# Kernel optimization log

Measured on AMD Instinct MI355X. Metric: run time of the kernel, lower is better.

Reference implementation:

```python
import jax, jax.numpy as jnp
import numpy as np


def setup_inputs() -> dict:
    key = jax.random.key(0)
    kx, kw = jax.random.split(key)
    x = jax.random.normal(kx, (32, 2048, 256), dtype=jnp.float32)
    W = jax.random.normal(kw, (1024, 256), dtype=jnp.float32)  # codebook [K, D]
    return {"x": x, "W": W}


def reference(x, W):
    D = W.shape[1]
    flat = x.reshape(-1, D)  # [N, D]
    # Squared Euclidean distances [N, K]; argmin is identical to cdist argmin.
    d2 = (
        jnp.sum(flat * flat, axis=1, keepdims=True)
        - 2.0 * (flat @ W.T)
        + jnp.sum(W * W, axis=1)
    )
    idx = jnp.argmin(d2, axis=1)  # [N]
    quant = W[idx].reshape(x.shape)  # direct gather == one-hot @ W
    # Straight-through estimator
    quantized = x + jax.lax.stop_gradient(quant - x)
    e_latent = jnp.mean((jax.lax.stop_gradient(quantized) - x) ** 2)
    q_latent = jnp.mean((quantized - jax.lax.stop_gradient(x)) ** 2)
    commitment_cost = 0.25
    loss = q_latent + commitment_cost * e_latent
    return quantized, loss, idx[:, None]
```

## Files before the change

kernel.cpp:

```cpp
#include <hip/hip_runtime.h>


#define NROWS    65536
#define DDIM     256
#define KCODES   1024
#define DEXT     512
#define ND_TOTAL 16777216

typedef __attribute__((ext_vector_type(8))) short bf16x8;
typedef __attribute__((ext_vector_type(4))) float floatx4;

__device__ __forceinline__ unsigned short f2bf(float f) {
    unsigned int u = __float_as_uint(f);
    return (unsigned short)((u + 0x7FFFu + ((u >> 16) & 1u)) >> 16);
}
__device__ __forceinline__ float bf2f(unsigned short h) {
    return __uint_as_float((unsigned int)h << 16);
}
__device__ __forceinline__ void split4(float4 v, ushort4* hi, ushort4* lo) {
    unsigned short hx = f2bf(v.x), hy = f2bf(v.y), hz = f2bf(v.z), hw = f2bf(v.w);
    *hi = make_ushort4(hx, hy, hz, hw);
    *lo = make_ushort4(f2bf(v.x - bf2f(hx)), f2bf(v.y - bf2f(hy)),
                       f2bf(v.z - bf2f(hz)), f2bf(v.w - bf2f(hw)));
}
__device__ __forceinline__ void async_copy16(void* lds, const void* g) {
    __builtin_amdgcn_global_load_lds(
        (const __attribute__((address_space(1))) unsigned int*)g,
        (__attribute__((address_space(3))) unsigned int*)lds, 16, 0, 0);
}

__device__ __forceinline__ void merge2(float& v1, int& k1, float& v2, int& k2,
                                       float o1, int ok1, float o2, int ok2) {
    bool aw = (v1 < o1) || (v1 == o1 && k1 < ok1);
    float ca = aw ? v2 : v1; int kca = aw ? k2 : k1;
    float cb = aw ? o1 : o2; int kcb = aw ? ok1 : ok2;
    float nv1 = aw ? v1 : o1; int nk1 = aw ? k1 : ok1;
    bool cw = (ca < cb) || (ca == cb && kca < kcb);
    v1 = nv1; k1 = nk1;
    v2 = cw ? ca : cb; k2 = cw ? kca : kcb;
}

__global__ void vq_prepw(const float* __restrict__ W, unsigned short* __restrict__ What,
                         float* __restrict__ w2, float* __restrict__ w2m,
                         float* __restrict__ lossws) {
    int k = blockIdx.x * 256 + threadIdx.x;
    if (k == 0) lossws[0] = 0.0f;
    if (k >= KCODES) return;
    const float4* wr = (const float4*)(W + (size_t)k * DDIM);
    unsigned short* hrow = What + (size_t)k * DEXT;
    float s = 0.0f;
    for (int i = 0; i < 64; ++i) {
        float4 v = wr[i];
        s = fmaf(v.x, v.x, s); s = fmaf(v.y, v.y, s);
        s = fmaf(v.z, v.z, s); s = fmaf(v.w, v.w, s);
        ushort4 hv, lv;
        split4(v, &hv, &lv);
        *(ushort4*)(hrow + i * 4) = hv;
        *(ushort4*)(hrow + 256 + i * 4) = lv;
    }
    w2[k] = s;
    w2m[k] = s - 256.0f;
}

__global__ void vq_convx(const float* __restrict__ x, unsigned short* Xhat) {
    int gid = blockIdx.x * 256 + threadIdx.x;
    int row = gid >> 6, q = gid & 63;
    float4 v = ((const float4*)x)[gid];
    ushort4 hv, lv;
    split4(v, &hv, &lv);
    unsigned short* r = Xhat + (size_t)row * DEXT;
    *(ushort4*)(r + q * 4) = hv;
    *(ushort4*)(r + 256 + q * 4) = lv;
}

__global__ __launch_bounds__(256, 2) void vq_main(
    const unsigned short* Xhat, const unsigned short* __restrict__ What,
    const float* __restrict__ x, const float* __restrict__ W,
    const float* __restrict__ w2, const float* __restrict__ w2m,
    float* qout, float* lossws, float* idx_out)
{
    __shared__ __align__(16) unsigned short smem[2 * 4 * 128 * 32];
    __shared__ float Wm[KCODES];

    float* rv1   = (float*)smem;
    float* rv2   = rv1 + 256;
    int*   rk1   = (int*)(rv2 + 256);
    int*   rk2   = rk1 + 256;
    int*   candk = rk2 + 256;
    float* resc  = (float*)(candk + 512);
    int*   fink  = (int*)(resc + 512);

    const int tid  = threadIdx.x;
    const int wave = tid >> 6, lane = tid & 63;
    const int quad = lane >> 4, l15 = lane & 15;
    const int wr = wave >> 1, wc = wave & 1;
    const int row0 = blockIdx.x * 128;

    #pragma unroll
    for (int t = 0; t < 4; ++t) Wm[t * 256 + tid] = w2m[t * 256 + tid];

    float s1[16], s2[16];
    #pragma unroll
    for (int s = 0; s < 16; ++s) { s1[s] = 3.0e38f; s2[s] = 3.0e38f; }

    const int r0 = tid >> 2, p0 = tid & 3;
    const int psw = (p0 ^ ((r0 >> 1) & 3)) << 3;
    const int quadS8 = (quad ^ ((l15 >> 1) & 3)) << 3;
    const unsigned short* Ab = Xhat + (size_t)row0 * DEXT;

    auto STAGE = [&](int q, int cb) {
        const int ct = q >> 3, dc = (q & 7) << 5;
        const unsigned short* An = Ab + (size_t)r0 * DEXT + dc + psw;
        const unsigned short* Bn = What + ((size_t)(ct * 128 + r0)) * DEXT + dc + psw;
        unsigned short* L = smem + cb * 16384 + tid * 8;
        async_copy16(L,          An);
        async_copy16(L + 2048,   An + 64 * DEXT);
        async_copy16(L + 4096,   An + 256);
        async_copy16(L + 6144,   An + 64 * DEXT + 256);
        async_copy16(L + 8192,   Bn);
        async_copy16(L + 10240,  Bn + 64 * DEXT);
        async_copy16(L + 12288,  Bn + 256);
        async_copy16(L + 14336,  Bn + 64 * DEXT + 256);
    };

    STAGE(0, 0);
    STAGE(1, 1);

    floatx4 acc[4][4];
    #pragma unroll
    for (int i = 0; i < 4; ++i)
        #pragma unroll
        for (int j = 0; j < 4; ++j) acc[i][j] = (floatx4){0.f, 0.f, 0.f, 0.f};

    #pragma unroll 1
    for (int q = 0; q < 64; ++q) {
        const int cb = q & 1;
        if (q != 63) { asm volatile("s_waitcnt vmcnt(8)" ::: "memory"); }
        else         { asm volatile("s_waitcnt vmcnt(0)" ::: "memory"); }
        __builtin_amdgcn_s_barrier();
        asm volatile("" ::: "memory");
        __builtin_amdgcn_s_setprio(1);

        const unsigned short* Sb = smem + cb * 16384;
        bf16x8 a0[4], a1[4], b0[4], b1[4];
        #pragma unroll
        for (int i = 0; i < 4; ++i) {
            const int ro = (wr * 64 + i * 16 + l15) * 32 + quadS8;
            a0[i] = *(const bf16x8*)(Sb + ro);
            a1[i] = *(const bf16x8*)(Sb + 4096 + ro);
        }
        #pragma unroll
        for (int j = 0; j < 4; ++j) {
            const int ro = (wc * 64 + j * 16 + l15) * 32 + quadS8;
            b0[j] = *(const bf16x8*)(Sb + 8192 + ro);
            b1[j] = *(const bf16x8*)(Sb + 12288 + ro);
        }
        #pragma unroll
        for (int i = 0; i < 4; ++i)
            #pragma unroll
            for (int j = 0; j < 4; ++j) {
                acc[i][j] = __builtin_amdgcn_mfma_f32_16x16x32_bf16(a0[i], b0[j], acc[i][j], 0, 0, 0);
                acc[i][j] = __builtin_amdgcn_mfma_f32_16x16x32_bf16(a1[i], b1[j], acc[i][j], 0, 0, 0);
                acc[i][j] = __builtin_amdgcn_mfma_f32_16x16x32_bf16(a0[i], b1[j], acc[i][j], 0, 0, 0);
                acc[i][j] = __builtin_amdgcn_mfma_f32_16x16x32_bf16(a1[i], b0[j], acc[i][j], 0, 0, 0);
            }
        __builtin_amdgcn_s_setprio(0);
        asm volatile("s_waitcnt lgkmcnt(0)" ::: "memory");
        __builtin_amdgcn_s_barrier();
        asm volatile("" ::: "memory");
        if (q + 2 < 64) STAGE(q + 2, cb);

        if ((q & 7) == 7) {
            const int ctf = q >> 3;
            #pragma unroll
            for (int j = 0; j < 4; ++j) {
                int cc = ctf * 128 + wc * 64 + j * 16 + l15;
                float wm = Wm[cc];
                unsigned pay = (unsigned)((j << 3) | ctf);
                #pragma unroll
                for (int i = 0; i < 4; ++i)
                    #pragma unroll
                    for (int r = 0; r < 4; ++r) {
                        float v = fmaf(-2.0f, acc[i][j][r], wm);
                        float pf = __uint_as_float((__float_as_uint(v) & 0xFFFFFFE0u) | pay);
                        int s = i * 4 + r;
                        float t = fminf(s1[s], pf);
                        s2[s] = fminf(s2[s], fmaxf(s1[s], pf));
                        s1[s] = t;
                    }
            }
            #pragma unroll
            for (int i = 0; i < 4; ++i)
                #pragma unroll
                for (int j = 0; j < 4; ++j) acc[i][j] = (floatx4){0.f, 0.f, 0.f, 0.f};
        }
    }

    float v1[16], v2[16];
    int k1[16], k2[16];
    #pragma unroll
    for (int s = 0; s < 16; ++s) {
        unsigned u1 = __float_as_uint(s1[s]) & 31u;
        unsigned u2 = __float_as_uint(s2[s]) & 31u;
        v1[s] = s1[s]; v2[s] = s2[s];
        k1[s] = (int)(u1 & 7u) * 128 + wc * 64 + (int)(u1 >> 3) * 16 + l15;
        k2[s] = (int)(u2 & 7u) * 128 + wc * 64 + (int)(u2 >> 3) * 16 + l15;
    }
    #pragma unroll
    for (int m = 1; m < 16; m <<= 1) {
        #pragma unroll
        for (int s = 0; s < 16; ++s) {
            float o1 = __shfl_xor(v1[s], m, 64);
            int  ok1 = __shfl_xor(k1[s], m, 64);
            float o2 = __shfl_xor(v2[s], m, 64);
            int  ok2 = __shfl_xor(k2[s], m, 64);
            merge2(v1[s], k1[s], v2[s], k2[s], o1, ok1, o2, ok2);
        }
    }
    if (l15 == 0) {
        #pragma unroll
        for (int s = 0; s < 16; ++s) {
            int row = wr * 64 + (s >> 2) * 16 + quad * 4 + (s & 3);
            rv1[wc * 128 + row] = v1[s]; rk1[wc * 128 + row] = k1[s];
            rv2[wc * 128 + row] = v2[s]; rk2[wc * 128 + row] = k2[s];
        }
    }
    __syncthreads();
    if (tid < 128) {
        candk[tid * 4 + 0] = rk1[tid];
        candk[tid * 4 + 1] = rk2[tid];
        candk[tid * 4 + 2] = rk1[128 + tid];
        candk[tid * 4 + 3] = rk2[128 + tid];
    }
    __syncthreads();
    #pragma unroll
    for (int j2 = 0; j2 < 2; ++j2) {
        int job = tid + j2 * 256;
        int r = job >> 2, cn = job & 3;
        int k = candk[r * 4 + cn];
        const float4* xr  = (const float4*)(x + (size_t)(row0 + r) * DDIM);
        const float4* wrp = (const float4*)(W + (size_t)k * DDIM);
        float dot = 0.0f;
        #pragma unroll 8
        for (int i = 0; i < 64; ++i) {
            float4 va = xr[i], vb = wrp[i];
            dot = fmaf(va.x, vb.x, dot); dot = fmaf(va.y, vb.y, dot);
            dot = fmaf(va.z, vb.z, dot); dot = fmaf(va.w, vb.w, dot);
        }
        resc[r * 4 + cn] = fmaf(-2.0f, dot, w2[k]);
    }
    __syncthreads();
    if (tid < 128) {
        float bd = resc[tid * 4 + 0];
        int   bk = candk[tid * 4 + 0];
        #pragma unroll
        for (int cn = 1; cn < 4; ++cn) {
            float d = resc[tid * 4 + cn];
            int   k = candk[tid * 4 + cn];
            if (d < bd || (d == bd && k < bk)) { bd = d; bk = k; }
        }
        fink[tid] = bk;
        idx_out[row0 + tid] = (float)bk;
    }
    __syncthreads();

    const int c4 = tid & 63, rsub = tid >> 6;
    float lsum = 0.0f;
    for (int it2 = 0; it2 < 32; ++it2) {
        int r = it2 * 4 + rsub;
        int k = fink[r];
        float4 wv = ((const float4*)(W + (size_t)k * DDIM))[c4];
        float4 xv = ((const float4*)(x + (size_t)(row0 + r) * DDIM))[c4];
        ((float4*)(qout + (size_t)(row0 + r) * DDIM))[c4] = wv;
        float dx = wv.x - xv.x, dy = wv.y - xv.y;
        float dz = wv.z - xv.z, dw = wv.w - xv.w;
        lsum = fmaf(dx, dx, lsum); lsum = fmaf(dy, dy, lsum);
        lsum = fmaf(dz, dz, lsum); lsum = fmaf(dw, dw, lsum);
    }
    #pragma unroll
    for (int off = 32; off > 0; off >>= 1) lsum += __shfl_down(lsum, off, 64);
    if (lane == 0) atomicAdd(lossws, lsum);
}

__global__ void vq_fin(const float* __restrict__ lossws, float* __restrict__ loss_out) {
    loss_out[0] = 1.25f * lossws[0] / (float)ND_TOTAL;
}

extern "C" void kernel_launch(void* const* d_in, const int* in_sizes, int n_in,
                              void* d_out, int out_size, void* d_ws, size_t ws_size,
                              hipStream_t stream) {
    const float* x = (const float*)d_in[0];
    const float* W = (const float*)d_in[1];
    float* out = (float*)d_out;
    unsigned short* Xhat = (unsigned short*)d_out;
    unsigned short* What = (unsigned short*)d_ws;
    float* w2     = (float*)((char*)d_ws + (1 << 20));
    float* w2m    = w2 + 1024;
    float* lossws = w2 + 2048;
    float* idx_out = out + (size_t)ND_TOTAL + 1;

    vq_prepw<<<4, 256, 0, stream>>>(W, What, w2, w2m, lossws);
    vq_convx<<<16384, 256, 0, stream>>>(x, Xhat);
    vq_main<<<512, 256, 0, stream>>>(Xhat, What, x, W, w2, w2m, out, lossws, idx_out);
    vq_fin<<<1, 1, 0, stream>>>(lossws, out + ND_TOTAL);
}
```

Measured before the change: 336.2 us.

## Widen main block to 512 threads with 256-code tiles and fuse prep kernels

After: 405.1 us. 1.21x slower.

```diff
diff --git a/kernel.cpp b/kernel.cpp
--- a/kernel.cpp
+++ b/kernel.cpp
@@ -40,64 +40,64 @@
     v2 = cw ? ca : cb; k2 = cw ? kca : kcb;
 }
 
-__global__ void vq_prepw(const float* __restrict__ W, unsigned short* __restrict__ What,
-                         float* __restrict__ w2, float* __restrict__ w2m,
-                         float* __restrict__ lossws) {
-    int k = blockIdx.x * 256 + threadIdx.x;
-    if (k == 0) lossws[0] = 0.0f;
-    if (k >= KCODES) return;
-    const float4* wr = (const float4*)(W + (size_t)k * DDIM);
-    unsigned short* hrow = What + (size_t)k * DEXT;
-    float s = 0.0f;
-    for (int i = 0; i < 64; ++i) {
-        float4 v = wr[i];
-        s = fmaf(v.x, v.x, s); s = fmaf(v.y, v.y, s);
-        s = fmaf(v.z, v.z, s); s = fmaf(v.w, v.w, s);
+__global__ __launch_bounds__(256) void vq_prep(
+    const float* __restrict__ x, unsigned short* __restrict__ Xhat,
+    const float* __restrict__ W, unsigned short* __restrict__ What,
+    float* __restrict__ w2, float* __restrict__ w2m, float* __restrict__ lossws)
+{
+    const int b = blockIdx.x;
+    if (b < 16384) {
+        int gid = b * 256 + threadIdx.x;
+        int row = gid >> 6, q = gid & 63;
+        float4 v = ((const float4*)x)[gid];
         ushort4 hv, lv;
         split4(v, &hv, &lv);
-        *(ushort4*)(hrow + i * 4) = hv;
-        *(ushort4*)(hrow + 256 + i * 4) = lv;
-    }
-    w2[k] = s;
-    w2m[k] = s - 256.0f;
-}
-
-__global__ void vq_convx(const float* __restrict__ x, unsigned short* Xhat) {
-    int gid = blockIdx.x * 256 + threadIdx.x;
-    int row = gid >> 6, q = gid & 63;
-    float4 v = ((const float4*)x)[gid];
-    ushort4 hv, lv;
-    split4(v, &hv, &lv);
-    unsigned short* r = Xhat + (size_t)row * DEXT;
-    *(ushort4*)(r + q * 4) = hv;
-    *(ushort4*)(r + 256 + q * 4) = lv;
-}
-
-__global__ __launch_bounds__(256, 2) void vq_main(
+        unsigned short* r = Xhat + (size_t)row * DEXT;
+        *(ushort4*)(r + q * 4) = hv;
+        *(ushort4*)(r + 256 + q * 4) = lv;
+    } else {
+        int k = (b - 16384) * 256 + threadIdx.x;
+        if (k == 0) lossws[0] = 0.0f;
+        const float4* wr = (const float4*)(W + (size_t)k * DDIM);
+        unsigned short* hrow = What + (size_t)k * DEXT;
+        float s = 0.0f;
+        for (int i = 0; i < 64; ++i) {
+            float4 v = wr[i];
+            s = fmaf(v.x, v.x, s); s = fmaf(v.y, v.y, s);
+            s = fmaf(v.z, v.z, s); s = fmaf(v.w, v.w, s);
+            ushort4 hv, lv;
+            split4(v, &hv, &lv);
+            *(ushort4*)(hrow + i * 4) = hv;
+            *(ushort4*)(hrow + 256 + i * 4) = lv;
+        }
+        w2[k] = s;
+        w2m[k] = s - 256.0f;
+    }
+}
+
+__global__ __launch_bounds__(512, 2) void vq_main(
     const unsigned short* Xhat, const unsigned short* __restrict__ What,
     const float* __restrict__ x, const float* __restrict__ W,
     const float* __restrict__ w2, const float* __restrict__ w2m,
     float* qout, float* lossws, float* idx_out)
 {
-    __shared__ __align__(16) unsigned short smem[2 * 4 * 128 * 32];
+    __shared__ __align__(16) unsigned short smem[2 * 24576];
     __shared__ float Wm[KCODES];
 
-    float* rv1   = (float*)smem;
-    float* rv2   = rv1 + 256;
-    int*   rk1   = (int*)(rv2 + 256);
-    int*   rk2   = rk1 + 256;
-    int*   candk = rk2 + 256;
-    float* resc  = (float*)(candk + 512);
-    int*   fink  = (int*)(resc + 512);
+    int*   rk1   = (int*)smem;
+    int*   rk2   = rk1 + 512;
+    int*   candk = rk2 + 512;
+    float* resc  = (float*)(candk + 1024);
+    int*   fink  = (int*)(resc + 1024);
 
     const int tid  = threadIdx.x;
     const int wave = tid >> 6, lane = tid & 63;
     const int quad = lane >> 4, l15 = lane & 15;
-    const int wr = wave >> 1, wc = wave & 1;
+    const int wr = wave >> 2, wc = wave & 3;
     const int row0 = blockIdx.x * 128;
 
-    #pragma unroll
-    for (int t = 0; t < 4; ++t) Wm[t * 256 + tid] = w2m[t * 256 + tid];
+    Wm[tid] = w2m[tid];
+    Wm[512 + tid] = w2m[512 + tid];
 
     float s1[16], s2[16];
     #pragma unroll
@@ -111,16 +111,14 @@
     auto STAGE = [&](int q, int cb) {
         const int ct = q >> 3, dc = (q & 7) << 5;
         const unsigned short* An = Ab + (size_t)r0 * DEXT + dc + psw;
-        const unsigned short* Bn = What + ((size_t)(ct * 128 + r0)) * DEXT + dc + psw;
-        unsigned short* L = smem + cb * 16384 + tid * 8;
+        const unsigned short* Bn = What + ((size_t)(ct * 256 + r0)) * DEXT + dc + psw;
+        unsigned short* L = smem + cb * 24576 + tid * 8;
         async_copy16(L,          An);
-        async_copy16(L + 2048,   An + 64 * DEXT);
         async_copy16(L + 4096,   An + 256);
-        async_copy16(L + 6144,   An + 64 * DEXT + 256);
         async_copy16(L + 8192,   Bn);
-        async_copy16(L + 10240,  Bn + 64 * DEXT);
-        async_copy16(L + 12288,  Bn + 256);
-        async_copy16(L + 14336,  Bn + 64 * DEXT + 256);
+        async_copy16(L + 12288,  Bn + 128 * DEXT);
+        async_copy16(L + 16384,  Bn + 256);
+        async_copy16(L + 20480,  Bn + 128 * DEXT + 256);
     };
 
     STAGE(0, 0);
@@ -133,15 +131,15 @@
         for (int j = 0; j < 4; ++j) acc[i][j] = (floatx4){0.f, 0.f, 0.f, 0.f};
 
     #pragma unroll 1
-    for (int q = 0; q < 64; ++q) {
+    for (int q = 0; q < 32; ++q) {
         const int cb = q & 1;
-        if (q != 63) { asm volatile("s_waitcnt vmcnt(8)" ::: "memory"); }
+        if (q != 31) { asm volatile("s_waitcnt vmcnt(6)" ::: "memory"); }
         else         { asm volatile("s_waitcnt vmcnt(0)" ::: "memory"); }
         __builtin_amdgcn_s_barrier();
         asm volatile("" ::: "memory");
         __builtin_amdgcn_s_setprio(1);
 
-        const unsigned short* Sb = smem + cb * 16384;
+        const unsigned short* Sb = smem + cb * 24576;
         bf16x8 a0[4], a1[4], b0[4], b1[4];
         #pragma unroll
         for (int i = 0; i < 4; ++i) {
@@ -153,7 +151,7 @@
         for (int j = 0; j < 4; ++j) {
             const int ro = (wc * 64 + j * 16 + l15) * 32 + quadS8;
             b0[j] = *(const bf16x8*)(Sb + 8192 + ro);
-            b1[j] = *(const bf16x8*)(Sb + 12288 + ro);
+            b1[j] = *(const bf16x8*)(Sb + 16384 + ro);
         }
         #pragma unroll
         for (int i = 0; i < 4; ++i)
@@ -168,21 +166,21 @@
         asm volatile("s_waitcnt lgkmcnt(0)" ::: "memory");
         __builtin_amdgcn_s_barrier();
         asm volatile("" ::: "memory");
-        if (q + 2 < 64) STAGE(q + 2, cb);
+        if (q + 2 < 32) STAGE(q + 2, cb);
 
         if ((q & 7) == 7) {
             const int ctf = q >> 3;
             #pragma unroll
             for (int j = 0; j < 4; ++j) {
-                int cc = ctf * 128 + wc * 64 + j * 16 + l15;
+                int cc = ctf * 256 + wc * 64 + j * 16 + l15;
                 float wm = Wm[cc];
-                unsigned pay = (unsigned)((j << 3) | ctf);
+                unsigned pay = (unsigned)((j << 2) | ctf);
                 #pragma unroll
                 for (int i = 0; i < 4; ++i)
                     #pragma unroll
                     for (int r = 0; r < 4; ++r) {
                         float v = fmaf(-2.0f, acc[i][j][r], wm);
-                        float pf = __uint_as_float((__float_as_uint(v) & 0xFFFFFFE0u) | pay);
+                        float pf = __uint_as_float((__float_as_uint(v) & 0xFFFFFFF0u) | pay);
                         int s = i * 4 + r;
                         float t = fminf(s1[s], pf);
                         s2[s] = fminf(s2[s], fmaxf(s1[s], pf));
@@ -200,11 +198,11 @@
     int k1[16], k2[16];
     #pragma unroll
     for (int s = 0; s < 16; ++s) {
-        unsigned u1 = __float_as_uint(s1[s]) & 31u;
-        unsigned u2 = __float_as_uint(s2[s]) & 31u;
+        unsigned u1 = __float_as_uint(s1[s]) & 15u;
+        unsigned u2 = __float_as_uint(s2[s]) & 15u;
         v1[s] = s1[s]; v2[s] = s2[s];
-        k1[s] = (int)(u1 & 7u) * 128 + wc * 64 + (int)(u1 >> 3) * 16 + l15;
-        k2[s] = (int)(u2 & 7u) * 128 + wc * 64 + (int)(u2 >> 3) * 16 + l15;
+        k1[s] = (int)(u1 & 3u) * 256 + wc * 64 + (int)(u1 >> 2) * 16 + l15;
+        k2[s] = (int)(u2 & 3u) * 256 + wc * 64 + (int)(u2 >> 2) * 16 + l15;
     }
     #pragma unroll
     for (int m = 1; m < 16; m <<= 1) {
@@ -221,23 +219,24 @@
         #pragma unroll
         for (int s = 0; s < 16; ++s) {
             int row = wr * 64 + (s >> 2) * 16 + quad * 4 + (s & 3);
-            rv1[wc * 128 + row] = v1[s]; rk1[wc * 128 + row] = k1[s];
-            rv2[wc * 128 + row] = v2[s]; rk2[wc * 128 + row] = k2[s];
+            rk1[wc * 128 + row] = k1[s];
+            rk2[wc * 128 + row] = k2[s];
         }
     }
     __syncthreads();
     if (tid < 128) {
-        candk[tid * 4 + 0] = rk1[tid];
-        candk[tid * 4 + 1] = rk2[tid];
-        candk[tid * 4 + 2] = rk1[128 + tid];
-        candk[tid * 4 + 3] = rk2[128 + tid];
+        #pragma unroll
+        for (int h = 0; h < 4; ++h) {
+            candk[tid * 8 + h * 2 + 0] = rk1[h * 128 + tid];
+            candk[tid * 8 + h * 2 + 1] = rk2[h * 128 + tid];
+        }
     }
     __syncthreads();
     #pragma unroll
     for (int j2 = 0; j2 < 2; ++j2) {
-        int job = tid + j2 * 256;
-        int r = job >> 2, cn = job & 3;
-        int k = candk[r * 4 + cn];
+        int job = tid + j2 * 512;
+        int r = job >> 3, cn = job & 7;
+        int k = candk[r * 8 + cn];
         const float4* xr  = (const float4*)(x + (size_t)(row0 + r) * DDIM);
         const float4* wrp = (const float4*)(W + (size_t)k * DDIM);
         float dot = 0.0f;
@@ -247,16 +246,16 @@
             dot = fmaf(va.x, vb.x, dot); dot = fmaf(va.y, vb.y, dot);
             dot = fmaf(va.z, vb.z, dot); dot = fmaf(va.w, vb.w, dot);
         }
-        resc[r * 4 + cn] = fmaf(-2.0f, dot, w2[k]);
+        resc[r * 8 + cn] = fmaf(-2.0f, dot, w2[k]);
     }
     __syncthreads();
     if (tid < 128) {
-        float bd = resc[tid * 4 + 0];
-        int   bk = candk[tid * 4 + 0];
-        #pragma unroll
-        for (int cn = 1; cn < 4; ++cn) {
-            float d = resc[tid * 4 + cn];
-            int   k = candk[tid * 4 + cn];
+        float bd = resc[tid * 8 + 0];
+        int   bk = candk[tid * 8 + 0];
+        #pragma unroll
+        for (int cn = 1; cn < 8; ++cn) {
+            float d = resc[tid * 8 + cn];
+            int   k = candk[tid * 8 + cn];
             if (d < bd || (d == bd && k < bk)) { bd = d; bk = k; }
         }
         fink[tid] = bk;
@@ -266,8 +265,8 @@
 
     const int c4 = tid & 63, rsub = tid >> 6;
     float lsum = 0.0f;
-    for (int it2 = 0; it2 < 32; ++it2) {
-        int r = it2 * 4 + rsub;
+    for (int it2 = 0; it2 < 16; ++it2) {
+        int r = it2 * 8 + rsub;
         int k = fink[r];
         float4 wv = ((const float4*)(W + (size_t)k * DDIM))[c4];
         float4 xv = ((const float4*)(x + (size_t)(row0 + r) * DDIM))[c4];
@@ -299,8 +298,7 @@
     float* lossws = w2 + 2048;
     float* idx_out = out + (size_t)ND_TOTAL + 1;
 
-    vq_prepw<<<4, 256, 0, stream>>>(W, What, w2, w2m, lossws);
-    vq_convx<<<16384, 256, 0, stream>>>(x, Xhat);
-    vq_main<<<512, 256, 0, stream>>>(Xhat, What, x, W, w2, w2m, out, lossws, idx_out);
+    vq_prep<<<16388, 256, 0, stream>>>(x, Xhat, W, What, w2, w2m, lossws);
+    vq_main<<<512, 512, 0, stream>>>(Xhat, What, x, W, w2, w2m, out, lossws, idx_out);
     vq_fin<<<1, 1, 0, stream>>>(lossws, out + ND_TOTAL);
 }
```

## Fuse x conversion and loss finalization into main kernel, simplify LDS pipeline

Applied to the files above, without the earlier changes.

Result: no change. 335.7 us (-0.2%).

```diff
diff --git a/kernel.cpp b/kernel.cpp
--- a/kernel.cpp
+++ b/kernel.cpp
@@ -40,12 +40,13 @@
     v2 = cw ? ca : cb; k2 = cw ? kca : kcb;
 }
 
-__global__ void vq_prepw(const float* __restrict__ W, unsigned short* __restrict__ What,
-                         float* __restrict__ w2, float* __restrict__ w2m,
-                         float* __restrict__ lossws) {
+__global__ __launch_bounds__(256) void vq_prepw(
+    const float* __restrict__ W, unsigned short* __restrict__ What,
+    float* __restrict__ w2, float* __restrict__ w2m,
+    float* __restrict__ lossws, unsigned* __restrict__ ticket)
+{
     int k = blockIdx.x * 256 + threadIdx.x;
-    if (k == 0) lossws[0] = 0.0f;
-    if (k >= KCODES) return;
+    if (k == 0) { lossws[0] = 0.0f; ticket[0] = 0u; }
     const float4* wr = (const float4*)(W + (size_t)k * DDIM);
     unsigned short* hrow = What + (size_t)k * DEXT;
     float s = 0.0f;
@@ -62,29 +63,16 @@
     w2m[k] = s - 256.0f;
 }
 
-__global__ void vq_convx(const float* __restrict__ x, unsigned short* Xhat) {
-    int gid = blockIdx.x * 256 + threadIdx.x;
-    int row = gid >> 6, q = gid & 63;
-    float4 v = ((const float4*)x)[gid];
-    ushort4 hv, lv;
-    split4(v, &hv, &lv);
-    unsigned short* r = Xhat + (size_t)row * DEXT;
-    *(ushort4*)(r + q * 4) = hv;
-    *(ushort4*)(r + 256 + q * 4) = lv;
-}
-
 __global__ __launch_bounds__(256, 2) void vq_main(
-    const unsigned short* Xhat, const unsigned short* __restrict__ What,
+    unsigned short* Xhat, const unsigned short* __restrict__ What,
     const float* __restrict__ x, const float* __restrict__ W,
     const float* __restrict__ w2, const float* __restrict__ w2m,
-    float* qout, float* lossws, float* idx_out)
+    float* qout, float* lossws, unsigned* ticket, float* loss_out, float* idx_out)
 {
-    __shared__ __align__(16) unsigned short smem[2 * 4 * 128 * 32];
+    __shared__ __align__(16) unsigned short smem[2 * 16384];
     __shared__ float Wm[KCODES];
 
-    float* rv1   = (float*)smem;
-    float* rv2   = rv1 + 256;
-    int*   rk1   = (int*)(rv2 + 256);
+    int*   rk1   = (int*)smem;
     int*   rk2   = rk1 + 256;
     int*   candk = rk2 + 256;
     float* resc  = (float*)(candk + 512);
@@ -99,6 +87,19 @@
     #pragma unroll
     for (int t = 0; t < 4; ++t) Wm[t * 256 + tid] = w2m[t * 256 + tid];
 
+    #pragma unroll 4
+    for (int it = 0; it < 32; ++it) {
+        int gid = it * 256 + tid;
+        int row = gid >> 6, qq = gid & 63;
+        float4 v = ((const float4*)(x + (size_t)(row0 + row) * DDIM))[qq];
+        ushort4 hv, lv;
+        split4(v, &hv, &lv);
+        unsigned short* r = Xhat + (size_t)(row0 + row) * DEXT;
+        *(ushort4*)(r + qq * 4) = hv;
+        *(ushort4*)(r + 256 + qq * 4) = lv;
+    }
+    __syncthreads();
+
     float s1[16], s2[16];
     #pragma unroll
     for (int s = 0; s < 16; ++s) { s1[s] = 3.0e38f; s2[s] = 3.0e38f; }
@@ -106,13 +107,14 @@
     const int r0 = tid >> 2, p0 = tid & 3;
     const int psw = (p0 ^ ((r0 >> 1) & 3)) << 3;
     const int quadS8 = (quad ^ ((l15 >> 1) & 3)) << 3;
-    const unsigned short* Ab = Xhat + (size_t)row0 * DEXT;
-
-    auto STAGE = [&](int q, int cb) {
+    const unsigned short* Abase = Xhat + (size_t)row0 * DEXT + (size_t)r0 * DEXT + psw;
+    const unsigned short* Bbase = What + (size_t)r0 * DEXT + psw;
+
+    auto STAGE = [&](int q) {
         const int ct = q >> 3, dc = (q & 7) << 5;
-        const unsigned short* An = Ab + (size_t)r0 * DEXT + dc + psw;
-        const unsigned short* Bn = What + ((size_t)(ct * 128 + r0)) * DEXT + dc + psw;
-        unsigned short* L = smem + cb * 16384 + tid * 8;
+        unsigned short* L = smem + (q & 1) * 16384 + tid * 8;
+        const unsigned short* An = Abase + dc;
+        const unsigned short* Bn = Bbase + (size_t)ct * 128 * DEXT + dc;
         async_copy16(L,          An);
         async_copy16(L + 2048,   An + 64 * DEXT);
         async_copy16(L + 4096,   An + 256);
@@ -123,8 +125,7 @@
         async_copy16(L + 14336,  Bn + 64 * DEXT + 256);
     };
 
-    STAGE(0, 0);
-    STAGE(1, 1);
+    STAGE(0);
 
     floatx4 acc[4][4];
     #pragma unroll
@@ -134,15 +135,13 @@
 
     #pragma unroll 1
     for (int q = 0; q < 64; ++q) {
-        const int cb = q & 1;
-        if (q != 63) { asm volatile("s_waitcnt vmcnt(8)" ::: "memory"); }
-        else         { asm volatile("s_waitcnt vmcnt(0)" ::: "memory"); }
+        asm volatile("s_waitcnt vmcnt(0)" ::: "memory");
         __builtin_amdgcn_s_barrier();
         asm volatile("" ::: "memory");
-        __builtin_amdgcn_s_setprio(1);
-
-        const unsigned short* Sb = smem + cb * 16384;
-        bf16x8 a0[4], a1[4], b0[4], b1[4];
+        if (q + 1 < 64) STAGE(q + 1);
+
+        const unsigned short* Sb = smem + (q & 1) * 16384;
+        bf16x8 a0[4], a1[4];
         #pragma unroll
         for (int i = 0; i < 4; ++i) {
             const int ro = (wr * 64 + i * 16 + l15) * 32 + quadS8;
@@ -152,23 +151,18 @@
         #pragma unroll
         for (int j = 0; j < 4; ++j) {
             const int ro = (wc * 64 + j * 16 + l15) * 32 + quadS8;
-            b0[j] = *(const bf16x8*)(Sb + 8192 + ro);
-            b1[j] = *(const bf16x8*)(Sb + 12288 + ro);
-        }
-        #pragma unroll
-        for (int i = 0; i < 4; ++i)
+            bf16x8 b0 = *(const bf16x8*)(Sb + 8192 + ro);
+            bf16x8 b1 = *(const bf16x8*)(Sb + 12288 + ro);
+            __builtin_amdgcn_s_setprio(1);
             #pragma unroll
-            for (int j = 0; j < 4; ++j) {
-                acc[i][j] = __builtin_amdgcn_mfma_f32_16x16x32_bf16(a0[i], b0[j], acc[i][j], 0, 0, 0);
-                acc[i][j] = __builtin_amdgcn_mfma_f32_16x16x32_bf16(a1[i], b1[j], acc[i][j], 0, 0, 0);
-                acc[i][j] = __builtin_amdgcn_mfma_f32_16x16x32_bf16(a0[i], b1[j], acc[i][j], 0, 0, 0);
-                acc[i][j] = __builtin_amdgcn_mfma_f32_16x16x32_bf16(a1[i], b0[j], acc[i][j], 0, 0, 0);
+            for (int i = 0; i < 4; ++i) {
+                acc[i][j] = __builtin_amdgcn_mfma_f32_16x16x32_bf16(a0[i], b0, acc[i][j], 0, 0, 0);
+                acc[i][j] = __builtin_amdgcn_mfma_f32_16x16x32_bf16(a1[i], b1, acc[i][j], 0, 0, 0);
+                acc[i][j] = __builtin_amdgcn_mfma_f32_16x16x32_bf16(a0[i], b1, acc[i][j], 0, 0, 0);
+                acc[i][j] = __builtin_amdgcn_mfma_f32_16x16x32_bf16(a1[i], b0, acc[i][j], 0, 0, 0);
             }
-        __builtin_amdgcn_s_setprio(0);
-        asm volatile("s_waitcnt lgkmcnt(0)" ::: "memory");
-        __builtin_amdgcn_s_barrier();
-        asm volatile("" ::: "memory");
-        if (q + 2 < 64) STAGE(q + 2, cb);
+            __builtin_amdgcn_s_setprio(0);
+        }
 
         if ((q & 7) == 7) {
             const int ctf = q >> 3;
@@ -221,8 +215,8 @@
         #pragma unroll
         for (int s = 0; s < 16; ++s) {
             int row = wr * 64 + (s >> 2) * 16 + quad * 4 + (s & 3);
-            rv1[wc * 128 + row] = v1[s]; rk1[wc * 128 + row] = k1[s];
-            rv2[wc * 128 + row] = v2[s]; rk2[wc * 128 + row] = k2[s];
+            rk1[wc * 128 + row] = k1[s];
+            rk2[wc * 128 + row] = k2[s];
         }
     }
     __syncthreads();
@@ -280,10 +274,16 @@
     #pragma unroll
     for (int off = 32; off > 0; off >>= 1) lsum += __shfl_down(lsum, off, 64);
     if (lane == 0) atomicAdd(lossws, lsum);
-}
-
-__global__ void vq_fin(const float* __restrict__ lossws, float* __restrict__ loss_out) {
-    loss_out[0] = 1.25f * lossws[0] / (float)ND_TOTAL;
+
+    __syncthreads();
+    if (tid == 0) {
+        __threadfence();
+        unsigned old = atomicAdd(ticket, 1u);
+        if (old == 511u) {
+            float total = atomicAdd(lossws, 0.0f);
+            loss_out[0] = 1.25f * total / (float)ND_TOTAL;
+        }
+    }
 }
 
 extern "C" void kernel_launch(void* const* d_in, const int* in_sizes, int n_in,
@@ -297,10 +297,11 @@
     float* w2     = (float*)((char*)d_ws + (1 << 20));
     float* w2m    = w2 + 1024;
     float* lossws = w2 + 2048;
-    float* idx_out = out + (size_t)ND_TOTAL + 1;
-
-    vq_prepw<<<4, 256, 0, stream>>>(W, What, w2, w2m, lossws);
-    vq_convx<<<16384, 256, 0, stream>>>(x, Xhat);
-    vq_main<<<512, 256, 0, stream>>>(Xhat, What, x, W, w2, w2m, out, lossws, idx_out);
-    vq_fin<<<1, 1, 0, stream>>>(lossws, out + ND_TOTAL);
-}
+    unsigned* ticket = (unsigned*)(w2 + 2049);
+    float* loss_out = out + (size_t)ND_TOTAL;
+    float* idx_out  = out + (size_t)ND_TOTAL + 1;
+
+    vq_prepw<<<4, 256, 0, stream>>>(W, What, w2, w2m, lossws, ticket);
+    vq_main<<<512, 256, 0, stream>>>(Xhat, What, x, W, w2, w2m, out,
+                                     lossws, ticket, loss_out, idx_out);
+}
```
